# Optimization experiments

Hardware: AMD Instinct MI355X
Metric: run time of the kernel (lower is better)

The kernel has to match this reference:

```python
import jax, jax.numpy as jnp
import numpy as np

D_MODEL = 1024
NUM_HEADS = 16
D_K = D_MODEL // NUM_HEADS
SCALE = np.sqrt(D_K).astype(np.float32)


def setup_inputs() -> dict:
    key = jax.random.key(0)
    ks = jax.random.split(key, 11)
    B, S, D = 2, 2048, D_MODEL
    std = 1.0 / np.sqrt(D)
    inp = {
        "Q": jax.random.normal(ks[0], (B, S, D), dtype=jnp.float32),
        "K": jax.random.normal(ks[1], (B, S, D), dtype=jnp.float32),
        "V": jax.random.normal(ks[2], (B, S, D), dtype=jnp.float32),
        "Wq": jax.random.normal(ks[3], (D, D), dtype=jnp.float32) * std,
        "bq": jnp.zeros((D,), dtype=jnp.float32),
        "Wk": jax.random.normal(ks[4], (D, D), dtype=jnp.float32) * std,
        "bk": jnp.zeros((D,), dtype=jnp.float32),
        "Wv": jax.random.normal(ks[5], (D, D), dtype=jnp.float32) * std,
        "bv": jnp.zeros((D,), dtype=jnp.float32),
        "Wo": jax.random.normal(ks[6], (D, D), dtype=jnp.float32) * std,
        "bo": jnp.zeros((D,), dtype=jnp.float32),
    }
    return inp


def reference(Q, K, V, Wq, bq, Wk, bk, Wv, bv, Wo, bo):
    B, S, D = Q.shape
    H, dk = NUM_HEADS, D_K
    # Linear projections then split heads: [B, S, D] -> [B, H, S, dk]
    def proj(x, W, b):
        y = x @ W.T + b
        return y.reshape(B, -1, H, dk).transpose(0, 2, 1, 3)
    q = proj(Q, Wq, bq)
    k = proj(K, Wk, bk)
    v = proj(V, Wv, bv)
    # scores: [B, H, S, S]
    scores = jnp.einsum("bhqd,bhkd->bhqk", q, k) / SCALE
    attn = jax.nn.softmax(scores, axis=-1)
    # dropout is identity in eval mode
    context = jnp.einsum("bhqk,bhkd->bhqd", attn, v)
    context = context.transpose(0, 2, 1, 3).reshape(B, -1, D)
    output = context @ Wo.T + bo
    return output, attn
```

## Files before the change

kernel.cpp:

```cpp
#include <hip/hip_runtime.h>
#include <stdint.h>

#define BB 2
#define SS 2048
#define DD 1024
#define HH 16
#define DKK 64

typedef unsigned short u16;
typedef short short8 __attribute__((ext_vector_type(8)));
typedef float f32x4 __attribute__((ext_vector_type(4)));
typedef u16 u16x4 __attribute__((ext_vector_type(4)));

#define QSCALE 0.18033688011112042f

__device__ __forceinline__ u16 f2bf(float x){
  union { float f; uint32_t u; } v; v.f = x;
  uint32_t r = v.u + 0x7FFFu + ((v.u >> 16) & 1u);
  return (u16)(r >> 16);
}

typedef __attribute__((address_space(1))) const void gv_t;
typedef __attribute__((address_space(3))) void lv_t;
__device__ __forceinline__ void gload_lds16(const u16* g, u16* l){
  __builtin_amdgcn_global_load_lds((gv_t*)g, (lv_t*)l, 16, 0, 0);
}

__global__ __launch_bounds__(256)
void cvt_kernel(const float* __restrict__ a0, const float* __restrict__ a1,
                const float* __restrict__ a2, const float* __restrict__ a3,
                u16* __restrict__ o0, u16* __restrict__ o1,
                u16* __restrict__ o2, u16* __restrict__ o3,
                int n0, int n1, int n2, int n3)
{
  const float* a; u16* o; int n4;
  switch (blockIdx.y) {
    case 0:  a=a0; o=o0; n4=n0; break;
    case 1:  a=a1; o=o1; n4=n1; break;
    case 2:  a=a2; o=o2; n4=n2; break;
    default: a=a3; o=o3; n4=n3; break;
  }
  int stride = gridDim.x * blockDim.x;
  for (int i = blockIdx.x*blockDim.x + threadIdx.x; i < n4; i += stride){
    float4 v = ((const float4*)a)[i];
    u16x4 h;
    h[0]=f2bf(v.x); h[1]=f2bf(v.y); h[2]=f2bf(v.z); h[3]=f2bf(v.w);
    ((u16x4*)o)[i] = h;
  }
}

struct ProjArgs {
  const u16* A;
  const u16* W;
  const float* bias;
  void* out;
  int mode;
  float oscale;
};

__global__ __launch_bounds__(256)
void proj_kernel(ProjArgs a0, ProjArgs a1, ProjArgs a2)
{
  ProjArgs pa = (blockIdx.z == 0) ? a0 : (blockIdx.z == 1 ? a1 : a2);
  const int K = 1024;
  __shared__ __align__(16) u16 As[128*32];
  __shared__ __align__(16) u16 Bs[128*32];

  int tid = threadIdx.x;
  int wid = tid >> 6, lane = tid & 63;
  int lg = lane >> 4, lr = lane & 15;
  int tm = blockIdx.x * 128, tn = blockIdx.y * 128;
  int wr = (wid >> 1) * 64, wc = (wid & 1) * 64;

  f32x4 acc[4][4];
  #pragma unroll
  for (int m=0;m<4;m++)
    #pragma unroll
    for (int n=0;n<4;n++){ f32x4 z = {0.f,0.f,0.f,0.f}; acc[m][n] = z; }

  int sr = tid >> 2;
  int sc = (tid & 3) * 8;
  const u16* ga0 = pa.A + (size_t)(tm + sr)*K + sc;
  const u16* ga1 = pa.A + (size_t)(tm + 64 + sr)*K + sc;
  const u16* gb0 = pa.W + (size_t)(tn + sr)*K + sc;
  const u16* gb1 = pa.W + (size_t)(tn + 64 + sr)*K + sc;
  u16* la0 = As + sr*32 + sc;
  u16* la1 = As + (64 + sr)*32 + sc;
  u16* lb0 = Bs + sr*32 + sc;
  u16* lb1 = Bs + (64 + sr)*32 + sc;

  for (int kt = 0; kt < K; kt += 32){
    gload_lds16(ga0 + kt, la0);
    gload_lds16(ga1 + kt, la1);
    gload_lds16(gb0 + kt, lb0);
    gload_lds16(gb1 + kt, lb1);
    __syncthreads();

    short8 af[4], bf[4];
    #pragma unroll
    for (int m=0;m<4;m++) af[m] = *(const short8*)(As + (wr + m*16 + lr)*32 + lg*8);
    #pragma unroll
    for (int n=0;n<4;n++) bf[n] = *(const short8*)(Bs + (wc + n*16 + lr)*32 + lg*8);
    #pragma unroll
    for (int m=0;m<4;m++)
      #pragma unroll
      for (int n=0;n<4;n++)
        acc[m][n] = __builtin_amdgcn_mfma_f32_16x16x32_bf16(af[m], bf[n], acc[m][n], 0,0,0);
    __syncthreads();
  }

  #pragma unroll
  for (int m=0;m<4;m++){
    #pragma unroll
    for (int n=0;n<4;n++){
      #pragma unroll
      for (int r=0;r<4;r++){
        int gm = tm + wr + m*16 + lg*4 + r;
        int gn = tn + wc + n*16 + lr;
        float v = (acc[m][n][r] + pa.bias[gn]) * pa.oscale;
        if (pa.mode == 3){
          ((float*)pa.out)[(size_t)gm*DD + gn] = v;
        } else {
          int b_ = gm >> 11, s_ = gm & 2047;
          int h_ = gn >> 6,  d_ = gn & 63;
          int bh = b_*HH + h_;
          u16 hv = f2bf(v);
          if (pa.mode == 0){
            ((u16*)pa.out)[((size_t)bh*SS + s_)*DKK + d_] = hv;
          } else if (pa.mode == 1){
            int c   = s_ >> 5;
            int lr2 = s_ & 15;
            int tl  = (s_ >> 4) & 1;
            int sub = tl*2 + (d_ >> 5);
            int lg2 = (d_ >> 3) & 3;
            int e   = d_ & 7;
            ((u16*)pa.out)[(((size_t)bh*64 + c)*4 + sub)*512 + (lg2*16 + lr2)*8 + e] = hv;
          } else {
            int c   = s_ >> 5;
            int lg2 = (s_ >> 3) & 3;
            int e   = s_ & 7;
            int dt  = d_ >> 4;
            int lr2 = d_ & 15;
            ((u16*)pa.out)[(((size_t)bh*64 + c)*4 + dt)*512 + (lg2*16 + lr2)*8 + e] = hv;
          }
        }
      }
    }
  }
}

__global__ __launch_bounds__(256, 3)
void attn_fused_kernel(const u16* __restrict__ qb, const u16* __restrict__ kf,
                       const u16* __restrict__ vf, float* __restrict__ attn_out,
                       u16* __restrict__ ctx)
{
  __shared__ __align__(16) u16 ptile[4][1280];
  __shared__ f32x4 accbuf[2][64][8];
  __shared__ float rsbuf[4][32];

  int tid = threadIdx.x;
  int w = tid >> 6, lane = tid & 63;
  int lg = lane >> 4, lr = lane & 15;
  int p = w >> 1, par = w & 1;
  int L  = blockIdx.x;
  int bh = (L & 7)*4 + ((L >> 3) & 3);
  int qg = ((L >> 5) << 1) + p;

  const u16* qp = qb + ((size_t)bh*SS + qg*32)*DKK;
  const u16* kp = kf + (size_t)bh*131072;
  const u16* vp = vf + (size_t)bh*131072;
  u16* myt = ptile[w];

  short8 qf[2][2];
  #pragma unroll
  for (int rt=0;rt<2;rt++){
    qf[rt][0] = *(const short8*)(qp + (rt*16+lr)*DKK + lg*8);
    qf[rt][1] = *(const short8*)(qp + (rt*16+lr)*DKK + 32 + lg*8);
  }

  f32x4 acc[2][4];
  #pragma unroll
  for (int rt=0;rt<2;rt++)
    #pragma unroll
    for (int dt=0;dt<4;dt++){ f32x4 z={0.f,0.f,0.f,0.f}; acc[rt][dt]=z; }
  float rsum[2] = {0.f, 0.f};

  short8 kc[4];
  #pragma unroll
  for (int s=0;s<4;s++)
    kc[s] = *(const short8*)(kp + ((size_t)par*4 + s)*512 + lane*8);

  for (int i=0;i<32;i++){
    int c = par + 2*i;
    short8 vc0 = *(const short8*)(vp + ((size_t)c*4 + 0)*512 + lane*8);
    short8 vc1 = *(const short8*)(vp + ((size_t)c*4 + 1)*512 + lane*8);
    short8 ka0=kc[0], ka1=kc[1], kb0=kc[2], kb1=kc[3];
    if (i < 31){
      #pragma unroll
      for (int s=0;s<4;s++)
        kc[s] = *(const short8*)(kp + ((size_t)(c+2)*4 + s)*512 + lane*8);
    }
    #pragma unroll
    for (int rt=0;rt<2;rt++){
      f32x4 sA = {0.f,0.f,0.f,0.f}, sB = {0.f,0.f,0.f,0.f};
      sA = __builtin_amdgcn_mfma_f32_16x16x32_bf16(ka0, qf[rt][0], sA, 0,0,0);
      sA = __builtin_amdgcn_mfma_f32_16x16x32_bf16(ka1, qf[rt][1], sA, 0,0,0);
      sB = __builtin_amdgcn_mfma_f32_16x16x32_bf16(kb0, qf[rt][0], sB, 0,0,0);
      sB = __builtin_amdgcn_mfma_f32_16x16x32_bf16(kb1, qf[rt][1], sB, 0,0,0);
      u16x4 hA, hB;
      #pragma unroll
      for (int r=0;r<4;r++){
        float pA = __builtin_exp2f(sA[r]);
        float pB = __builtin_exp2f(sB[r]);
        rsum[rt] += pA + pB;
        hA[r] = f2bf(pA);
        hB[r] = f2bf(pB);
      }
      *(u16x4*)(myt + (rt*16+lr)*40 + lg*4)      = hA;
      *(u16x4*)(myt + (rt*16+lr)*40 + 16 + lg*4) = hB;
    }
    short8 vc2 = *(const short8*)(vp + ((size_t)c*4 + 2)*512 + lane*8);
    short8 vc3 = *(const short8*)(vp + ((size_t)c*4 + 3)*512 + lane*8);
    #pragma unroll
    for (int rt=0;rt<2;rt++){
      short8 pa = *(const short8*)(myt + (rt*16+lr)*40 + lg*8);
      acc[rt][0] = __builtin_amdgcn_mfma_f32_16x16x32_bf16(pa, vc0, acc[rt][0], 0,0,0);
      acc[rt][1] = __builtin_amdgcn_mfma_f32_16x16x32_bf16(pa, vc1, acc[rt][1], 0,0,0);
      acc[rt][2] = __builtin_amdgcn_mfma_f32_16x16x32_bf16(pa, vc2, acc[rt][2], 0,0,0);
      acc[rt][3] = __builtin_amdgcn_mfma_f32_16x16x32_bf16(pa, vc3, acc[rt][3], 0,0,0);
    }
  }

  #pragma unroll
  for (int rt=0;rt<2;rt++){
    float v = rsum[rt];
    v += __shfl_xor(v, 16);
    v += __shfl_xor(v, 32);
    if (lg == 0) rsbuf[w][rt*16 + lr] = v;
  }
  if (par == 1){
    #pragma unroll
    for (int rt=0;rt<2;rt++)
      #pragma unroll
      for (int dt=0;dt<4;dt++)
        accbuf[p][lane][rt*4+dt] = acc[rt][dt];
  }
  __syncthreads();

  float il[2];
  #pragma unroll
  for (int rt=0;rt<2;rt++)
    il[rt] = 1.0f / (rsbuf[p*2][rt*16 + lr] + rsbuf[p*2+1][rt*16 + lr]);

  if (par == 0){
    int b_ = bh >> 4, h_ = bh & 15;
    #pragma unroll
    for (int rt=0;rt<2;rt++){
      #pragma unroll
      for (int dt=0;dt<4;dt++)
        acc[rt][dt] += accbuf[p][lane][rt*4+dt];
      #pragma unroll
      for (int r=0;r<4;r++){
        float ilr = __shfl(il[rt], lg*4 + r, 16);
        int row = qg*32 + rt*16 + lg*4 + r;
        #pragma unroll
        for (int dt=0;dt<4;dt++){
          float vv = acc[rt][dt][r] * ilr;
          ctx[((size_t)b_*SS + row)*DD + h_*DKK + dt*16 + lr] = f2bf(vv);
        }
      }
    }
  }

  #pragma unroll
  for (int s=0;s<4;s++)
    kc[s] = *(const short8*)(kp + ((size_t)par*4 + s)*512 + lane*8);
  float* arow0 = attn_out + ((size_t)bh*SS + qg*32 + lr)*SS;
  float* arow1 = attn_out + ((size_t)bh*SS + qg*32 + 16 + lr)*SS;
  for (int i=0;i<32;i++){
    int c = par + 2*i;
    short8 ka0=kc[0], ka1=kc[1], kb0=kc[2], kb1=kc[3];
    if (i < 31){
      #pragma unroll
      for (int s=0;s<4;s++)
        kc[s] = *(const short8*)(kp + ((size_t)(c+2)*4 + s)*512 + lane*8);
    }
    #pragma unroll
    for (int rt=0;rt<2;rt++){
      f32x4 sA = {0.f,0.f,0.f,0.f}, sB = {0.f,0.f,0.f,0.f};
      sA = __builtin_amdgcn_mfma_f32_16x16x32_bf16(ka0, qf[rt][0], sA, 0,0,0);
      sA = __builtin_amdgcn_mfma_f32_16x16x32_bf16(ka1, qf[rt][1], sA, 0,0,0);
      sB = __builtin_amdgcn_mfma_f32_16x16x32_bf16(kb0, qf[rt][0], sB, 0,0,0);
      sB = __builtin_amdgcn_mfma_f32_16x16x32_bf16(kb1, qf[rt][1], sB, 0,0,0);
      float myil = il[rt];
      f32x4 oA, oB;
      #pragma unroll
      for (int r=0;r<4;r++){
        oA[r] = __builtin_exp2f(sA[r]) * myil;
        oB[r] = __builtin_exp2f(sB[r]) * myil;
      }
      float* arow = (rt == 0) ? arow0 : arow1;
      *(f32x4*)(arow + c*32 + lg*4)      = oA;
      *(f32x4*)(arow + c*32 + 16 + lg*4) = oB;
    }
  }
}

extern "C" void kernel_launch(void* const* d_in, const int* in_sizes, int n_in,
                              void* d_out, int out_size, void* d_ws, size_t ws_size,
                              hipStream_t stream)
{
  const float* Q   = (const float*)d_in[0];
  const float* Kin = (const float*)d_in[1];
  const float* V   = (const float*)d_in[2];
  const float* Wq  = (const float*)d_in[3];
  const float* bq  = (const float*)d_in[4];
  const float* Wk  = (const float*)d_in[5];
  const float* bk  = (const float*)d_in[6];
  const float* Wv  = (const float*)d_in[7];
  const float* bv  = (const float*)d_in[8];
  const float* Wo  = (const float*)d_in[9];
  const float* bo  = (const float*)d_in[10];

  char* ws = (char*)d_ws;
  u16* QB  = (u16*)(ws + (size_t)( 0u<<20));
  u16* KB  = (u16*)(ws + (size_t)( 8u<<20));
  u16* VB  = (u16*)(ws + (size_t)(16u<<20));
  u16* WQB = (u16*)(ws + (size_t)(24u<<20));
  u16* WKB = (u16*)(ws + (size_t)(26u<<20));
  u16* WVB = (u16*)(ws + (size_t)(28u<<20));
  u16* WOB = (u16*)(ws + (size_t)(30u<<20));
  u16* qh  = (u16*)(ws + (size_t)(32u<<20));
  u16* kfb = (u16*)(ws + (size_t)(40u<<20));
  u16* vfb = (u16*)(ws + (size_t)(48u<<20));
  u16* ctx = (u16*)(ws + (size_t)(56u<<20));

  float* out0     = (float*)d_out;
  float* attn_out = out0 + (size_t)BB*SS*DD;

  int n_qkv = (BB*SS*DD)/4;
  int n_w   = (DD*DD)/4;

  cvt_kernel<<<dim3(512,4), 256, 0, stream>>>(Q, Kin, V, Wq, QB, KB, VB, WQB,
                                              n_qkv, n_qkv, n_qkv, n_w);
  cvt_kernel<<<dim3(256,3), 256, 0, stream>>>(Wk, Wv, Wo, Wo, WKB, WVB, WOB, WOB,
                                              n_w, n_w, n_w, 0);

  ProjArgs pq = { QB, WQB, bq, qh,   0, QSCALE };
  ProjArgs pk = { KB, WKB, bk, kfb,  1, 1.0f   };
  ProjArgs pv = { VB, WVB, bv, vfb,  2, 1.0f   };
  ProjArgs po = { ctx, WOB, bo, out0, 3, 1.0f  };

  proj_kernel<<<dim3(32,8,3), 256, 0, stream>>>(pq, pk, pv);
  attn_fused_kernel<<<dim3(1024), 256, 0, stream>>>(qh, kfb, vfb, attn_out, ctx);
  proj_kernel<<<dim3(32,8,1), 256, 0, stream>>>(po, po, po);
}
```

Baseline: 270.4 us.

## Software-pipeline attention loop: overlap QK MFMA with previous tile's PV and exp

```diff
diff --git a/kernel.cpp b/kernel.cpp
--- a/kernel.cpp
+++ b/kernel.cpp
@@ -185,28 +185,26 @@
     for (int dt=0;dt<4;dt++){ f32x4 z={0.f,0.f,0.f,0.f}; acc[rt][dt]=z; }
   float rsum[2] = {0.f, 0.f};
 
-  short8 kc[4];
+  short8 kc[4], kn[4], vprev[4], vcur[4];
   #pragma unroll
   for (int s=0;s<4;s++)
     kc[s] = *(const short8*)(kp + ((size_t)par*4 + s)*512 + lane*8);
 
-  for (int i=0;i<32;i++){
-    int c = par + 2*i;
-    short8 vc0 = *(const short8*)(vp + ((size_t)c*4 + 0)*512 + lane*8);
-    short8 vc1 = *(const short8*)(vp + ((size_t)c*4 + 1)*512 + lane*8);
-    short8 ka0=kc[0], ka1=kc[1], kb0=kc[2], kb1=kc[3];
-    if (i < 31){
-      #pragma unroll
-      for (int s=0;s<4;s++)
-        kc[s] = *(const short8*)(kp + ((size_t)(c+2)*4 + s)*512 + lane*8);
-    }
+  {
+    int c = par;
+    #pragma unroll
+    for (int s=0;s<4;s++)
+      kn[s] = *(const short8*)(kp + ((size_t)(c+2)*4 + s)*512 + lane*8);
+    #pragma unroll
+    for (int dt=0;dt<4;dt++)
+      vprev[dt] = *(const short8*)(vp + ((size_t)c*4 + dt)*512 + lane*8);
     #pragma unroll
     for (int rt=0;rt<2;rt++){
       f32x4 sA = {0.f,0.f,0.f,0.f}, sB = {0.f,0.f,0.f,0.f};
-      sA = __builtin_amdgcn_mfma_f32_16x16x32_bf16(ka0, qf[rt][0], sA, 0,0,0);
-      sA = __builtin_amdgcn_mfma_f32_16x16x32_bf16(ka1, qf[rt][1], sA, 0,0,0);
-      sB = __builtin_amdgcn_mfma_f32_16x16x32_bf16(kb0, qf[rt][0], sB, 0,0,0);
-      sB = __builtin_amdgcn_mfma_f32_16x16x32_bf16(kb1, qf[rt][1], sB, 0,0,0);
+      sA = __builtin_amdgcn_mfma_f32_16x16x32_bf16(kc[0], qf[rt][0], sA, 0,0,0);
+      sA = __builtin_amdgcn_mfma_f32_16x16x32_bf16(kc[1], qf[rt][1], sA, 0,0,0);
+      sB = __builtin_amdgcn_mfma_f32_16x16x32_bf16(kc[2], qf[rt][0], sB, 0,0,0);
+      sB = __builtin_amdgcn_mfma_f32_16x16x32_bf16(kc[3], qf[rt][1], sB, 0,0,0);
       u16x4 hA, hB;
       #pragma unroll
       for (int r=0;r<4;r++){
@@ -219,16 +217,69 @@
       *(u16x4*)(myt + (rt*16+lr)*40 + lg*4)      = hA;
       *(u16x4*)(myt + (rt*16+lr)*40 + 16 + lg*4) = hB;
     }
-    short8 vc2 = *(const short8*)(vp + ((size_t)c*4 + 2)*512 + lane*8);
-    short8 vc3 = *(const short8*)(vp + ((size_t)c*4 + 3)*512 + lane*8);
+    #pragma unroll
+    for (int s=0;s<4;s++) kc[s] = kn[s];
+  }
+
+  for (int i=1;i<32;i++){
+    int c = par + 2*i;
+    if (i < 31){
+      #pragma unroll
+      for (int s=0;s<4;s++)
+        kn[s] = *(const short8*)(kp + ((size_t)(c+2)*4 + s)*512 + lane*8);
+    }
+    #pragma unroll
+    for (int dt=0;dt<4;dt++)
+      vcur[dt] = *(const short8*)(vp + ((size_t)c*4 + dt)*512 + lane*8);
+
+    f32x4 sA[2], sB[2];
+    #pragma unroll
+    for (int rt=0;rt<2;rt++){
+      f32x4 zA = {0.f,0.f,0.f,0.f}, zB = {0.f,0.f,0.f,0.f};
+      zA = __builtin_amdgcn_mfma_f32_16x16x32_bf16(kc[0], qf[rt][0], zA, 0,0,0);
+      zA = __builtin_amdgcn_mfma_f32_16x16x32_bf16(kc[1], qf[rt][1], zA, 0,0,0);
+      zB = __builtin_amdgcn_mfma_f32_16x16x32_bf16(kc[2], qf[rt][0], zB, 0,0,0);
+      zB = __builtin_amdgcn_mfma_f32_16x16x32_bf16(kc[3], qf[rt][1], zB, 0,0,0);
+      sA[rt] = zA; sB[rt] = zB;
+    }
+
     #pragma unroll
     for (int rt=0;rt<2;rt++){
       short8 pa = *(const short8*)(myt + (rt*16+lr)*40 + lg*8);
-      acc[rt][0] = __builtin_amdgcn_mfma_f32_16x16x32_bf16(pa, vc0, acc[rt][0], 0,0,0);
-      acc[rt][1] = __builtin_amdgcn_mfma_f32_16x16x32_bf16(pa, vc1, acc[rt][1], 0,0,0);
-      acc[rt][2] = __builtin_amdgcn_mfma_f32_16x16x32_bf16(pa, vc2, acc[rt][2], 0,0,0);
-      acc[rt][3] = __builtin_amdgcn_mfma_f32_16x16x32_bf16(pa, vc3, acc[rt][3], 0,0,0);
-    }
+      acc[rt][0] = __builtin_amdgcn_mfma_f32_16x16x32_bf16(pa, vprev[0], acc[rt][0], 0,0,0);
+      acc[rt][1] = __builtin_amdgcn_mfma_f32_16x16x32_bf16(pa, vprev[1], acc[rt][1], 0,0,0);
+      acc[rt][2] = __builtin_amdgcn_mfma_f32_16x16x32_bf16(pa, vprev[2], acc[rt][2], 0,0,0);
+      acc[rt][3] = __builtin_amdgcn_mfma_f32_16x16x32_bf16(pa, vprev[3], acc[rt][3], 0,0,0);
+    }
+
+    #pragma unroll
+    for (int rt=0;rt<2;rt++){
+      u16x4 hA, hB;
+      #pragma unroll
+      for (int r=0;r<4;r++){
+        float pA = __builtin_exp2f(sA[rt][r]);
+        float pB = __builtin_exp2f(sB[rt][r]);
+        rsum[rt] += pA + pB;
+        hA[r] = f2bf(pA);
+        hB[r] = f2bf(pB);
+      }
+      *(u16x4*)(myt + (rt*16+lr)*40 + lg*4)      = hA;
+      *(u16x4*)(myt + (rt*16+lr)*40 + 16 + lg*4) = hB;
+    }
+
+    #pragma unroll
+    for (int dt=0;dt<4;dt++) vprev[dt] = vcur[dt];
+    #pragma unroll
+    for (int s=0;s<4;s++) kc[s] = kn[s];
+  }
+
+  #pragma unroll
+  for (int rt=0;rt<2;rt++){
+    short8 pa = *(const short8*)(myt + (rt*16+lr)*40 + lg*8);
+    acc[rt][0] = __builtin_amdgcn_mfma_f32_16x16x32_bf16(pa, vprev[0], acc[rt][0], 0,0,0);
+    acc[rt][1] = __builtin_amdgcn_mfma_f32_16x16x32_bf16(pa, vprev[1], acc[rt][1], 0,0,0);
+    acc[rt][2] = __builtin_amdgcn_mfma_f32_16x16x32_bf16(pa, vprev[2], acc[rt][2], 0,0,0);
+    acc[rt][3] = __builtin_amdgcn_mfma_f32_16x16x32_bf16(pa, vprev[3], acc[rt][3], 0,0,0);
   }
 
   #pragma unroll
```

After: 274.9 us. About the same (+1.7%).

## Give each wave its own 16-row query strip over all keys in attention

Applied to the files above, without the earlier changes.

```diff
diff --git a/kernel.cpp b/kernel.cpp
--- a/kernel.cpp
+++ b/kernel.cpp
@@ -149,160 +149,115 @@
   }
 }
 
-__global__ __launch_bounds__(256, 3)
+__global__ __launch_bounds__(256)
 void attn_fused_kernel(const u16* __restrict__ qb, const u16* __restrict__ kf,
                        const u16* __restrict__ vf, float* __restrict__ attn_out,
                        u16* __restrict__ ctx)
 {
-  __shared__ __align__(16) u16 ptile[4][1280];
-  __shared__ f32x4 accbuf[2][64][8];
-  __shared__ float rsbuf[4][32];
+  __shared__ __align__(16) u16 ptile[4][640];
 
   int tid = threadIdx.x;
   int w = tid >> 6, lane = tid & 63;
   int lg = lane >> 4, lr = lane & 15;
-  int p = w >> 1, par = w & 1;
   int L  = blockIdx.x;
   int bh = (L & 7)*4 + ((L >> 3) & 3);
-  int qg = ((L >> 5) << 1) + p;
-
-  const u16* qp = qb + ((size_t)bh*SS + qg*32)*DKK;
+  int qs = (L >> 5)*4 + w;
+
+  const u16* qp = qb + ((size_t)bh*SS + qs*16)*DKK;
   const u16* kp = kf + (size_t)bh*131072;
   const u16* vp = vf + (size_t)bh*131072;
   u16* myt = ptile[w];
 
-  short8 qf[2][2];
-  #pragma unroll
-  for (int rt=0;rt<2;rt++){
-    qf[rt][0] = *(const short8*)(qp + (rt*16+lr)*DKK + lg*8);
-    qf[rt][1] = *(const short8*)(qp + (rt*16+lr)*DKK + 32 + lg*8);
-  }
-
-  f32x4 acc[2][4];
-  #pragma unroll
-  for (int rt=0;rt<2;rt++)
-    #pragma unroll
-    for (int dt=0;dt<4;dt++){ f32x4 z={0.f,0.f,0.f,0.f}; acc[rt][dt]=z; }
-  float rsum[2] = {0.f, 0.f};
+  short8 qf0 = *(const short8*)(qp + lr*DKK + lg*8);
+  short8 qf1 = *(const short8*)(qp + lr*DKK + 32 + lg*8);
+
+  f32x4 acc[4];
+  #pragma unroll
+  for (int dt=0;dt<4;dt++){ f32x4 z={0.f,0.f,0.f,0.f}; acc[dt]=z; }
+  float rsum = 0.f;
 
   short8 kc[4];
   #pragma unroll
   for (int s=0;s<4;s++)
-    kc[s] = *(const short8*)(kp + ((size_t)par*4 + s)*512 + lane*8);
-
-  for (int i=0;i<32;i++){
-    int c = par + 2*i;
+    kc[s] = *(const short8*)(kp + (size_t)s*512 + lane*8);
+
+  for (int c=0;c<64;c++){
     short8 vc0 = *(const short8*)(vp + ((size_t)c*4 + 0)*512 + lane*8);
     short8 vc1 = *(const short8*)(vp + ((size_t)c*4 + 1)*512 + lane*8);
     short8 ka0=kc[0], ka1=kc[1], kb0=kc[2], kb1=kc[3];
-    if (i < 31){
+    if (c < 63){
       #pragma unroll
       for (int s=0;s<4;s++)
-        kc[s] = *(const short8*)(kp + ((size_t)(c+2)*4 + s)*512 + lane*8);
-    }
-    #pragma unroll
-    for (int rt=0;rt<2;rt++){
-      f32x4 sA = {0.f,0.f,0.f,0.f}, sB = {0.f,0.f,0.f,0.f};
-      sA = __builtin_amdgcn_mfma_f32_16x16x32_bf16(ka0, qf[rt][0], sA, 0,0,0);
-      sA = __builtin_amdgcn_mfma_f32_16x16x32_bf16(ka1, qf[rt][1], sA, 0,0,0);
-      sB = __builtin_amdgcn_mfma_f32_16x16x32_bf16(kb0, qf[rt][0], sB, 0,0,0);
-      sB = __builtin_amdgcn_mfma_f32_16x16x32_bf16(kb1, qf[rt][1], sB, 0,0,0);
-      u16x4 hA, hB;
-      #pragma unroll
-      for (int r=0;r<4;r++){
-        float pA = __builtin_exp2f(sA[r]);
-        float pB = __builtin_exp2f(sB[r]);
-        rsum[rt] += pA + pB;
-        hA[r] = f2bf(pA);
-        hB[r] = f2bf(pB);
-      }
-      *(u16x4*)(myt + (rt*16+lr)*40 + lg*4)      = hA;
-      *(u16x4*)(myt + (rt*16+lr)*40 + 16 + lg*4) = hB;
-    }
+        kc[s] = *(const short8*)(kp + ((size_t)(c+1)*4 + s)*512 + lane*8);
+    }
+    f32x4 sA = {0.f,0.f,0.f,0.f}, sB = {0.f,0.f,0.f,0.f};
+    sA = __builtin_amdgcn_mfma_f32_16x16x32_bf16(ka0, qf0, sA, 0,0,0);
+    sA = __builtin_amdgcn_mfma_f32_16x16x32_bf16(ka1, qf1, sA, 0,0,0);
+    sB = __builtin_amdgcn_mfma_f32_16x16x32_bf16(kb0, qf0, sB, 0,0,0);
+    sB = __builtin_amdgcn_mfma_f32_16x16x32_bf16(kb1, qf1, sB, 0,0,0);
+    u16x4 hA, hB;
+    #pragma unroll
+    for (int r=0;r<4;r++){
+      float pA = __builtin_exp2f(sA[r]);
+      float pB = __builtin_exp2f(sB[r]);
+      rsum += pA + pB;
+      hA[r] = f2bf(pA);
+      hB[r] = f2bf(pB);
+    }
+    *(u16x4*)(myt + lr*40 + lg*4)      = hA;
+    *(u16x4*)(myt + lr*40 + 16 + lg*4) = hB;
     short8 vc2 = *(const short8*)(vp + ((size_t)c*4 + 2)*512 + lane*8);
     short8 vc3 = *(const short8*)(vp + ((size_t)c*4 + 3)*512 + lane*8);
-    #pragma unroll
-    for (int rt=0;rt<2;rt++){
-      short8 pa = *(const short8*)(myt + (rt*16+lr)*40 + lg*8);
-      acc[rt][0] = __builtin_amdgcn_mfma_f32_16x16x32_bf16(pa, vc0, acc[rt][0], 0,0,0);
-      acc[rt][1] = __builtin_amdgcn_mfma_f32_16x16x32_bf16(pa, vc1, acc[rt][1], 0,0,0);
-      acc[rt][2] = __builtin_amdgcn_mfma_f32_16x16x32_bf16(pa, vc2, acc[rt][2], 0,0,0);
-      acc[rt][3] = __builtin_amdgcn_mfma_f32_16x16x32_bf16(pa, vc3, acc[rt][3], 0,0,0);
-    }
-  }
-
-  #pragma unroll
-  for (int rt=0;rt<2;rt++){
-    float v = rsum[rt];
-    v += __shfl_xor(v, 16);
-    v += __shfl_xor(v, 32);
-    if (lg == 0) rsbuf[w][rt*16 + lr] = v;
-  }
-  if (par == 1){
-    #pragma unroll
-    for (int rt=0;rt<2;rt++)
-      #pragma unroll
-      for (int dt=0;dt<4;dt++)
-        accbuf[p][lane][rt*4+dt] = acc[rt][dt];
-  }
-  __syncthreads();
-
-  float il[2];
-  #pragma unroll
-  for (int rt=0;rt<2;rt++)
-    il[rt] = 1.0f / (rsbuf[p*2][rt*16 + lr] + rsbuf[p*2+1][rt*16 + lr]);
-
-  if (par == 0){
+    short8 pa = *(const short8*)(myt + lr*40 + lg*8);
+    acc[0] = __builtin_amdgcn_mfma_f32_16x16x32_bf16(pa, vc0, acc[0], 0,0,0);
+    acc[1] = __builtin_amdgcn_mfma_f32_16x16x32_bf16(pa, vc1, acc[1], 0,0,0);
+    acc[2] = __builtin_amdgcn_mfma_f32_16x16x32_bf16(pa, vc2, acc[2], 0,0,0);
+    acc[3] = __builtin_amdgcn_mfma_f32_16x16x32_bf16(pa, vc3, acc[3], 0,0,0);
+  }
+
+  float v = rsum;
+  v += __shfl_xor(v, 16);
+  v += __shfl_xor(v, 32);
+  float il = 1.0f / v;
+
+  {
     int b_ = bh >> 4, h_ = bh & 15;
     #pragma unroll
-    for (int rt=0;rt<2;rt++){
-      #pragma unroll
-      for (int dt=0;dt<4;dt++)
-        acc[rt][dt] += accbuf[p][lane][rt*4+dt];
-      #pragma unroll
-      for (int r=0;r<4;r++){
-        float ilr = __shfl(il[rt], lg*4 + r, 16);
-        int row = qg*32 + rt*16 + lg*4 + r;
-        #pragma unroll
-        for (int dt=0;dt<4;dt++){
-          float vv = acc[rt][dt][r] * ilr;
-          ctx[((size_t)b_*SS + row)*DD + h_*DKK + dt*16 + lr] = f2bf(vv);
-        }
+    for (int r=0;r<4;r++){
+      float ilr = __shfl(il, lg*4 + r, 16);
+      int row = qs*16 + lg*4 + r;
+      #pragma unroll
+      for (int dt=0;dt<4;dt++){
+        float vv = acc[dt][r] * ilr;
+        ctx[((size_t)b_*SS + row)*DD + h_*DKK + dt*16 + lr] = f2bf(vv);
       }
     }
   }
 
   #pragma unroll
   for (int s=0;s<4;s++)
-    kc[s] = *(const short8*)(kp + ((size_t)par*4 + s)*512 + lane*8);
-  float* arow0 = attn_out + ((size_t)bh*SS + qg*32 + lr)*SS;
-  float* arow1 = attn_out + ((size_t)bh*SS + qg*32 + 16 + lr)*SS;
-  for (int i=0;i<32;i++){
-    int c = par + 2*i;
+    kc[s] = *(const short8*)(kp + (size_t)s*512 + lane*8);
+  float* arow = attn_out + ((size_t)bh*SS + qs*16 + lr)*SS;
+  for (int c=0;c<64;c++){
     short8 ka0=kc[0], ka1=kc[1], kb0=kc[2], kb1=kc[3];
-    if (i < 31){
+    if (c < 63){
       #pragma unroll
       for (int s=0;s<4;s++)
-        kc[s] = *(const short8*)(kp + ((size_t)(c+2)*4 + s)*512 + lane*8);
-    }
-    #pragma unroll
-    for (int rt=0;rt<2;rt++){
-      f32x4 sA = {0.f,0.f,0.f,0.f}, sB = {0.f,0.f,0.f,0.f};
-      sA = __builtin_amdgcn_mfma_f32_16x16x32_bf16(ka0, qf[rt][0], sA, 0,0,0);
-      sA = __builtin_amdgcn_mfma_f32_16x16x32_bf16(ka1, qf[rt][1], sA, 0,0,0);
-      sB = __builtin_amdgcn_mfma_f32_16x16x32_bf16(kb0, qf[rt][0], sB, 0,0,0);
-      sB = __builtin_amdgcn_mfma_f32_16x16x32_bf16(kb1, qf[rt][1], sB, 0,0,0);
-      float myil = il[rt];
-      f32x4 oA, oB;
-      #pragma unroll
-      for (int r=0;r<4;r++){
-        oA[r] = __builtin_exp2f(sA[r]) * myil;
-        oB[r] = __builtin_exp2f(sB[r]) * myil;
-      }
-      float* arow = (rt == 0) ? arow0 : arow1;
-      *(f32x4*)(arow + c*32 + lg*4)      = oA;
-      *(f32x4*)(arow + c*32 + 16 + lg*4) = oB;
-    }
+        kc[s] = *(const short8*)(kp + ((size_t)(c+1)*4 + s)*512 + lane*8);
+    }
+    f32x4 sA = {0.f,0.f,0.f,0.f}, sB = {0.f,0.f,0.f,0.f};
+    sA = __builtin_amdgcn_mfma_f32_16x16x32_bf16(ka0, qf0, sA, 0,0,0);
+    sA = __builtin_amdgcn_mfma_f32_16x16x32_bf16(ka1, qf1, sA, 0,0,0);
+    sB = __builtin_amdgcn_mfma_f32_16x16x32_bf16(kb0, qf0, sB, 0,0,0);
+    sB = __builtin_amdgcn_mfma_f32_16x16x32_bf16(kb1, qf1, sB, 0,0,0);
+    f32x4 oA, oB;
+    #pragma unroll
+    for (int r=0;r<4;r++){
+      oA[r] = __builtin_exp2f(sA[r]) * il;
+      oB[r] = __builtin_exp2f(sB[r]) * il;
+    }
+    *(f32x4*)(arow + c*32 + lg*4)      = oA;
+    *(f32x4*)(arow + c*32 + 16 + lg*4) = oB;
   }
 }
 
```

New measurement: 303.4 us. +12.2%, slower.

## Stagger row tiles so attn writes of tile 0 overlap PV pass of tile 1

Applied to the files above, without the earlier changes.

```diff
diff --git a/kernel.cpp b/kernel.cpp
--- a/kernel.cpp
+++ b/kernel.cpp
@@ -154,9 +154,9 @@
                        const u16* __restrict__ vf, float* __restrict__ attn_out,
                        u16* __restrict__ ctx)
 {
-  __shared__ __align__(16) u16 ptile[4][1280];
-  __shared__ f32x4 accbuf[2][64][8];
-  __shared__ float rsbuf[4][32];
+  __shared__ __align__(16) u16 ptile[4][640];
+  __shared__ f32x4 accbuf[2][2][64][4];
+  __shared__ float rsbuf[2][4][16];
 
   int tid = threadIdx.x;
   int w = tid >> 6, lane = tid & 63;
@@ -170,6 +170,7 @@
   const u16* kp = kf + (size_t)bh*131072;
   const u16* vp = vf + (size_t)bh*131072;
   u16* myt = ptile[w];
+  int b_ = bh >> 4, h_ = bh & 15;
 
   short8 qf[2][2];
   #pragma unroll
@@ -178,12 +179,10 @@
     qf[rt][1] = *(const short8*)(qp + (rt*16+lr)*DKK + 32 + lg*8);
   }
 
-  f32x4 acc[2][4];
-  #pragma unroll
-  for (int rt=0;rt<2;rt++)
-    #pragma unroll
-    for (int dt=0;dt<4;dt++){ f32x4 z={0.f,0.f,0.f,0.f}; acc[rt][dt]=z; }
-  float rsum[2] = {0.f, 0.f};
+  f32x4 acc[4];
+  #pragma unroll
+  for (int dt=0;dt<4;dt++){ f32x4 z={0.f,0.f,0.f,0.f}; acc[dt]=z; }
+  float rsum = 0.f;
 
   short8 kc[4];
   #pragma unroll
@@ -200,82 +199,148 @@
       for (int s=0;s<4;s++)
         kc[s] = *(const short8*)(kp + ((size_t)(c+2)*4 + s)*512 + lane*8);
     }
-    #pragma unroll
-    for (int rt=0;rt<2;rt++){
-      f32x4 sA = {0.f,0.f,0.f,0.f}, sB = {0.f,0.f,0.f,0.f};
-      sA = __builtin_amdgcn_mfma_f32_16x16x32_bf16(ka0, qf[rt][0], sA, 0,0,0);
-      sA = __builtin_amdgcn_mfma_f32_16x16x32_bf16(ka1, qf[rt][1], sA, 0,0,0);
-      sB = __builtin_amdgcn_mfma_f32_16x16x32_bf16(kb0, qf[rt][0], sB, 0,0,0);
-      sB = __builtin_amdgcn_mfma_f32_16x16x32_bf16(kb1, qf[rt][1], sB, 0,0,0);
-      u16x4 hA, hB;
-      #pragma unroll
-      for (int r=0;r<4;r++){
-        float pA = __builtin_exp2f(sA[r]);
-        float pB = __builtin_exp2f(sB[r]);
-        rsum[rt] += pA + pB;
-        hA[r] = f2bf(pA);
-        hB[r] = f2bf(pB);
-      }
-      *(u16x4*)(myt + (rt*16+lr)*40 + lg*4)      = hA;
-      *(u16x4*)(myt + (rt*16+lr)*40 + 16 + lg*4) = hB;
-    }
+    f32x4 sA = {0.f,0.f,0.f,0.f}, sB = {0.f,0.f,0.f,0.f};
+    sA = __builtin_amdgcn_mfma_f32_16x16x32_bf16(ka0, qf[0][0], sA, 0,0,0);
+    sA = __builtin_amdgcn_mfma_f32_16x16x32_bf16(ka1, qf[0][1], sA, 0,0,0);
+    sB = __builtin_amdgcn_mfma_f32_16x16x32_bf16(kb0, qf[0][0], sB, 0,0,0);
+    sB = __builtin_amdgcn_mfma_f32_16x16x32_bf16(kb1, qf[0][1], sB, 0,0,0);
+    u16x4 hA, hB;
+    #pragma unroll
+    for (int r=0;r<4;r++){
+      float pA = __builtin_exp2f(sA[r]);
+      float pB = __builtin_exp2f(sB[r]);
+      rsum += pA + pB;
+      hA[r] = f2bf(pA);
+      hB[r] = f2bf(pB);
+    }
+    *(u16x4*)(myt + lr*40 + lg*4)      = hA;
+    *(u16x4*)(myt + lr*40 + 16 + lg*4) = hB;
     short8 vc2 = *(const short8*)(vp + ((size_t)c*4 + 2)*512 + lane*8);
     short8 vc3 = *(const short8*)(vp + ((size_t)c*4 + 3)*512 + lane*8);
-    #pragma unroll
-    for (int rt=0;rt<2;rt++){
-      short8 pa = *(const short8*)(myt + (rt*16+lr)*40 + lg*8);
-      acc[rt][0] = __builtin_amdgcn_mfma_f32_16x16x32_bf16(pa, vc0, acc[rt][0], 0,0,0);
-      acc[rt][1] = __builtin_amdgcn_mfma_f32_16x16x32_bf16(pa, vc1, acc[rt][1], 0,0,0);
-      acc[rt][2] = __builtin_amdgcn_mfma_f32_16x16x32_bf16(pa, vc2, acc[rt][2], 0,0,0);
-      acc[rt][3] = __builtin_amdgcn_mfma_f32_16x16x32_bf16(pa, vc3, acc[rt][3], 0,0,0);
-    }
-  }
-
-  #pragma unroll
-  for (int rt=0;rt<2;rt++){
-    float v = rsum[rt];
+    short8 pa = *(const short8*)(myt + lr*40 + lg*8);
+    acc[0] = __builtin_amdgcn_mfma_f32_16x16x32_bf16(pa, vc0, acc[0], 0,0,0);
+    acc[1] = __builtin_amdgcn_mfma_f32_16x16x32_bf16(pa, vc1, acc[1], 0,0,0);
+    acc[2] = __builtin_amdgcn_mfma_f32_16x16x32_bf16(pa, vc2, acc[2], 0,0,0);
+    acc[3] = __builtin_amdgcn_mfma_f32_16x16x32_bf16(pa, vc3, acc[3], 0,0,0);
+  }
+
+  {
+    float v = rsum;
     v += __shfl_xor(v, 16);
     v += __shfl_xor(v, 32);
-    if (lg == 0) rsbuf[w][rt*16 + lr] = v;
+    if (lg == 0) rsbuf[0][w][lr] = v;
   }
   if (par == 1){
     #pragma unroll
-    for (int rt=0;rt<2;rt++)
-      #pragma unroll
-      for (int dt=0;dt<4;dt++)
-        accbuf[p][lane][rt*4+dt] = acc[rt][dt];
+    for (int dt=0;dt<4;dt++) accbuf[0][p][lane][dt] = acc[dt];
   }
   __syncthreads();
-
-  float il[2];
-  #pragma unroll
-  for (int rt=0;rt<2;rt++)
-    il[rt] = 1.0f / (rsbuf[p*2][rt*16 + lr] + rsbuf[p*2+1][rt*16 + lr]);
+  float il0 = 1.0f / (rsbuf[0][p*2][lr] + rsbuf[0][p*2+1][lr]);
 
   if (par == 0){
-    int b_ = bh >> 4, h_ = bh & 15;
-    #pragma unroll
-    for (int rt=0;rt<2;rt++){
-      #pragma unroll
-      for (int dt=0;dt<4;dt++)
-        acc[rt][dt] += accbuf[p][lane][rt*4+dt];
-      #pragma unroll
-      for (int r=0;r<4;r++){
-        float ilr = __shfl(il[rt], lg*4 + r, 16);
-        int row = qg*32 + rt*16 + lg*4 + r;
-        #pragma unroll
-        for (int dt=0;dt<4;dt++){
-          float vv = acc[rt][dt][r] * ilr;
-          ctx[((size_t)b_*SS + row)*DD + h_*DKK + dt*16 + lr] = f2bf(vv);
-        }
+    #pragma unroll
+    for (int dt=0;dt<4;dt++) acc[dt] += accbuf[0][p][lane][dt];
+    #pragma unroll
+    for (int r=0;r<4;r++){
+      float ilr = __shfl(il0, lg*4 + r, 16);
+      int row = qg*32 + lg*4 + r;
+      #pragma unroll
+      for (int dt=0;dt<4;dt++){
+        float vv = acc[dt][r] * ilr;
+        ctx[((size_t)b_*SS + row)*DD + h_*DKK + dt*16 + lr] = f2bf(vv);
       }
     }
   }
 
+  #pragma unroll
+  for (int dt=0;dt<4;dt++){ f32x4 z={0.f,0.f,0.f,0.f}; acc[dt]=z; }
+  rsum = 0.f;
   #pragma unroll
   for (int s=0;s<4;s++)
     kc[s] = *(const short8*)(kp + ((size_t)par*4 + s)*512 + lane*8);
   float* arow0 = attn_out + ((size_t)bh*SS + qg*32 + lr)*SS;
+
+  for (int i=0;i<32;i++){
+    int c = par + 2*i;
+    short8 vc0 = *(const short8*)(vp + ((size_t)c*4 + 0)*512 + lane*8);
+    short8 vc1 = *(const short8*)(vp + ((size_t)c*4 + 1)*512 + lane*8);
+    short8 ka0=kc[0], ka1=kc[1], kb0=kc[2], kb1=kc[3];
+    if (i < 31){
+      #pragma unroll
+      for (int s=0;s<4;s++)
+        kc[s] = *(const short8*)(kp + ((size_t)(c+2)*4 + s)*512 + lane*8);
+    }
+    {
+      f32x4 s0A = {0.f,0.f,0.f,0.f}, s0B = {0.f,0.f,0.f,0.f};
+      s0A = __builtin_amdgcn_mfma_f32_16x16x32_bf16(ka0, qf[0][0], s0A, 0,0,0);
+      s0A = __builtin_amdgcn_mfma_f32_16x16x32_bf16(ka1, qf[0][1], s0A, 0,0,0);
+      s0B = __builtin_amdgcn_mfma_f32_16x16x32_bf16(kb0, qf[0][0], s0B, 0,0,0);
+      s0B = __builtin_amdgcn_mfma_f32_16x16x32_bf16(kb1, qf[0][1], s0B, 0,0,0);
+      f32x4 oA, oB;
+      #pragma unroll
+      for (int r=0;r<4;r++){
+        oA[r] = __builtin_exp2f(s0A[r]) * il0;
+        oB[r] = __builtin_exp2f(s0B[r]) * il0;
+      }
+      *(f32x4*)(arow0 + c*32 + lg*4)      = oA;
+      *(f32x4*)(arow0 + c*32 + 16 + lg*4) = oB;
+    }
+    f32x4 sA = {0.f,0.f,0.f,0.f}, sB = {0.f,0.f,0.f,0.f};
+    sA = __builtin_amdgcn_mfma_f32_16x16x32_bf16(ka0, qf[1][0], sA, 0,0,0);
+    sA = __builtin_amdgcn_mfma_f32_16x16x32_bf16(ka1, qf[1][1], sA, 0,0,0);
+    sB = __builtin_amdgcn_mfma_f32_16x16x32_bf16(kb0, qf[1][0], sB, 0,0,0);
+    sB = __builtin_amdgcn_mfma_f32_16x16x32_bf16(kb1, qf[1][1], sB, 0,0,0);
+    u16x4 hA, hB;
+    #pragma unroll
+    for (int r=0;r<4;r++){
+      float pA = __builtin_exp2f(sA[r]);
+      float pB = __builtin_exp2f(sB[r]);
+      rsum += pA + pB;
+      hA[r] = f2bf(pA);
+      hB[r] = f2bf(pB);
+    }
+    *(u16x4*)(myt + lr*40 + lg*4)      = hA;
+    *(u16x4*)(myt + lr*40 + 16 + lg*4) = hB;
+    short8 vc2 = *(const short8*)(vp + ((size_t)c*4 + 2)*512 + lane*8);
+    short8 vc3 = *(const short8*)(vp + ((size_t)c*4 + 3)*512 + lane*8);
+    short8 pa = *(const short8*)(myt + lr*40 + lg*8);
+    acc[0] = __builtin_amdgcn_mfma_f32_16x16x32_bf16(pa, vc0, acc[0], 0,0,0);
+    acc[1] = __builtin_amdgcn_mfma_f32_16x16x32_bf16(pa, vc1, acc[1], 0,0,0);
+    acc[2] = __builtin_amdgcn_mfma_f32_16x16x32_bf16(pa, vc2, acc[2], 0,0,0);
+    acc[3] = __builtin_amdgcn_mfma_f32_16x16x32_bf16(pa, vc3, acc[3], 0,0,0);
+  }
+
+  {
+    float v = rsum;
+    v += __shfl_xor(v, 16);
+    v += __shfl_xor(v, 32);
+    if (lg == 0) rsbuf[1][w][lr] = v;
+  }
+  if (par == 1){
+    #pragma unroll
+    for (int dt=0;dt<4;dt++) accbuf[1][p][lane][dt] = acc[dt];
+  }
+  __syncthreads();
+  float il1 = 1.0f / (rsbuf[1][p*2][lr] + rsbuf[1][p*2+1][lr]);
+
+  if (par == 0){
+    #pragma unroll
+    for (int dt=0;dt<4;dt++) acc[dt] += accbuf[1][p][lane][dt];
+    #pragma unroll
+    for (int r=0;r<4;r++){
+      float ilr = __shfl(il1, lg*4 + r, 16);
+      int row = qg*32 + 16 + lg*4 + r;
+      #pragma unroll
+      for (int dt=0;dt<4;dt++){
+        float vv = acc[dt][r] * ilr;
+        ctx[((size_t)b_*SS + row)*DD + h_*DKK + dt*16 + lr] = f2bf(vv);
+      }
+    }
+  }
+
+  #pragma unroll
+  for (int s=0;s<4;s++)
+    kc[s] = *(const short8*)(kp + ((size_t)par*4 + s)*512 + lane*8);
   float* arow1 = attn_out + ((size_t)bh*SS + qg*32 + 16 + lr)*SS;
   for (int i=0;i<32;i++){
     int c = par + 2*i;
@@ -285,24 +350,19 @@
       for (int s=0;s<4;s++)
         kc[s] = *(const short8*)(kp + ((size_t)(c+2)*4 + s)*512 + lane*8);
     }
-    #pragma unroll
-    for (int rt=0;rt<2;rt++){
-      f32x4 sA = {0.f,0.f,0.f,0.f}, sB = {0.f,0.f,0.f,0.f};
-      sA = __builtin_amdgcn_mfma_f32_16x16x32_bf16(ka0, qf[rt][0], sA, 0,0,0);
-      sA = __builtin_amdgcn_mfma_f32_16x16x32_bf16(ka1, qf[rt][1], sA, 0,0,0);
-      sB = __builtin_amdgcn_mfma_f32_16x16x32_bf16(kb0, qf[rt][0], sB, 0,0,0);
-      sB = __builtin_amdgcn_mfma_f32_16x16x32_bf16(kb1, qf[rt][1], sB, 0,0,0);
-      float myil = il[rt];
-      f32x4 oA, oB;
-      #pragma unroll
-      for (int r=0;r<4;r++){
-        oA[r] = __builtin_exp2f(sA[r]) * myil;
-        oB[r] = __builtin_exp2f(sB[r]) * myil;
-      }
-      float* arow = (rt == 0) ? arow0 : arow1;
-      *(f32x4*)(arow + c*32 + lg*4)      = oA;
-      *(f32x4*)(arow + c*32 + 16 + lg*4) = oB;
-    }
+    f32x4 sA = {0.f,0.f,0.f,0.f}, sB = {0.f,0.f,0.f,0.f};
+    sA = __builtin_amdgcn_mfma_f32_16x16x32_bf16(ka0, qf[1][0], sA, 0,0,0);
+    sA = __builtin_amdgcn_mfma_f32_16x16x32_bf16(ka1, qf[1][1], sA, 0,0,0);
+    sB = __builtin_amdgcn_mfma_f32_16x16x32_bf16(kb0, qf[1][0], sB, 0,0,0);
+    sB = __builtin_amdgcn_mfma_f32_16x16x32_bf16(kb1, qf[1][1], sB, 0,0,0);
+    f32x4 oA, oB;
+    #pragma unroll
+    for (int r=0;r<4;r++){
+      oA[r] = __builtin_exp2f(sA[r]) * il1;
+      oB[r] = __builtin_exp2f(sB[r]) * il1;
+    }
+    *(f32x4*)(arow1 + c*32 + lg*4)      = oA;
+    *(f32x4*)(arow1 + c*32 + 16 + lg*4) = oB;
   }
 }
 
```

Result: slower. 289.9 us (+7.2%).
